# Kernel optimization log

Hardware: AMD Instinct MI355X
Metric: run time of the kernel (lower is better)

## Reference

```python
import jax, jax.numpy as jnp
import numpy as np

MEAN_STOP_TIME_S = 60.0
MIN_ROUTE_LEN = 2
DEMAND_TIME_WEIGHT = 0.5
ROUTE_TIME_WEIGHT = 0.5
UNSERVED_WEIGHT = 5.0

B, N, R, L, K = 64, 512, 40, 20, 4


def setup_inputs() -> dict:
    key = jax.random.key(0)
    ks = jax.random.split(key, 8)
    demand = jax.random.uniform(ks[0], (B, N, N), dtype=jnp.float32) * 10.0
    drive_times = jax.random.uniform(ks[1], (B, N, N), dtype=jnp.float32) * 1800.0
    transit_times = jax.random.uniform(ks[2], (B, N, N), dtype=jnp.float32) * 3600.0
    has_path = jax.random.randint(ks[3], (B, N, N), 0, 2) > 0
    n_transfers = jax.random.randint(ks[4], (B, N, N), 0, 4).astype(jnp.int32)
    # routes with -1 padding past a random per-route length
    routes = jax.random.randint(ks[5], (B, R, L), 0, N).astype(jnp.int32)
    lens = jax.random.randint(ks[6], (B, R), 0, L + 1)
    valid = jnp.arange(L)[None, None, :] < lens[:, :, None]
    batch_routes = jnp.where(valid, routes, -1)
    # per demand-edge route assignments, -1 = unused slot
    route_seqs = (jax.random.randint(ks[7], (B, N, N, K), 0, R + 1) - 1).astype(jnp.int32)
    return {
        'demand': demand, 'drive_times': drive_times, 'transit_times': transit_times,
        'has_path': has_path, 'n_transfers': n_transfers,
        'batch_routes': batch_routes, 'route_seqs': route_seqs,
    }


def _route_leg_times(batch_routes, dtm, mean_stop_time_s):
    # leg (l -> l+1) of each route: dtm[b, from, to] + stop time, masked on valid stops
    frm = batch_routes[:, :, :-1]
    to = batch_routes[:, :, 1:]
    valid = (frm >= 0) & (to >= 0)
    bidx = jnp.arange(dtm.shape[0])[:, None, None]
    times = dtm[bidx, jnp.maximum(frm, 0), jnp.maximum(to, 0)] + mean_stop_time_s
    return jnp.where(valid, times, 0.0)  # [B, R, L-1]


def _per_route_riders(demand, route_seqs, n_routes):
    # segment-sum demand over route ids; -1 slots go to a dump bucket
    def per_b(dem, rs):
        ids = rs.reshape(-1)
        vals = jnp.broadcast_to(dem[..., None], rs.shape).reshape(-1)
        ids = jnp.where(ids < 0, n_routes, ids)
        return jax.ops.segment_sum(vals, ids, num_segments=n_routes + 1)[:n_routes]
    return jax.vmap(per_b)(demand, route_seqs)  # [B, R]


def reference(demand, drive_times, transit_times, has_path, n_transfers,
              batch_routes, route_seqs):
    fdem = demand
    nopath = ~has_path
    route_lens = (batch_routes > -1).sum(-1)  # [B, R]

    n_disconnected = (nopath & (fdem > 0)).sum(axis=(1, 2))
    route_len_delta = jnp.maximum(MIN_ROUTE_LEN - route_lens, 0)
    route_len_delta = jnp.where(route_lens == 0, 0, route_len_delta)
    n_stops_oob = route_len_delta.sum(-1)  # [B]

    nt_eff = jnp.where(nopath, 3, n_transfers)
    tat = jnp.stack([
        (fdem * (nt_eff == 0)).sum(axis=(1, 2)),
        (fdem * (nt_eff == 1)).sum(axis=(1, 2)),
        (fdem * (nt_eff == 2)).sum(axis=(1, 2)),
        (fdem * (nt_eff > 2)).sum(axis=(1, 2)),
    ], axis=-1)  # trips_at_transfers [B, 4]

    trip_times = jnp.where(nopath, 0.0, transit_times)
    total_dmd_time = (fdem * trip_times).sum(axis=(1, 2))
    total_transfers = (fdem * n_transfers.astype(fdem.dtype)).sum(axis=(1, 2))
    unserved = (fdem * nopath).sum(axis=(1, 2))
    total_demand = fdem.sum(axis=(1, 2))

    leg_times = _route_leg_times(batch_routes, drive_times, MEAN_STOP_TIME_S)
    total_route_time = leg_times.sum(axis=(1, 2))
    # symmetric_routes=True: add return-direction legs
    ret = _route_leg_times(batch_routes, jnp.swapaxes(drive_times, 1, 2), MEAN_STOP_TIME_S)
    total_route_time = total_route_time + ret.sum(axis=(1, 2))

    per_route_riders = _per_route_riders(fdem, route_seqs, R)

    # cost assembly
    time_norm = drive_times.max(axis=(1, 2))
    served = total_demand - unserved
    mean_dmd_time = total_dmd_time / (served + 1e-6)
    norm_dmd_time = mean_dmd_time / time_norm
    n_routes_used = (route_lens > 0).sum(-1)
    norm_route_time = total_route_time / (time_norm * n_routes_used + 1e-6)
    n_demand_edges = (fdem > 0).sum(axis=(1, 2))
    frac_uncovered = n_disconnected / n_demand_edges
    denom = n_routes_used * MIN_ROUTE_LEN
    frac_oob = n_stops_oob / (denom + 1e-6)
    cost = (DEMAND_TIME_WEIGHT * norm_dmd_time
            + ROUTE_TIME_WEIGHT * norm_route_time
            + UNSERVED_WEIGHT * (frac_uncovered + frac_oob))
    return cost, per_route_riders, tat, total_route_time


if __name__ == '__main__':
    out = reference(**setup_inputs())
    print([o.shape for o in out])
```

## Files before the change

kernel.cpp:

```cpp
#include <hip/hip_runtime.h>

#define NB 64
#define NDIM 512
#define NNE (NDIM * NDIM)
#define NR 40
#define NL 20
#define SUBS 16
#define IT 16
#define BINS 41

#define K1OFF 0
#define K1STRIDE 16
#define K2OFF (NB * SUBS * K1STRIDE)
#define K3OFF (K2OFF + NB * SUBS)
#define K3STRIDE 48
#define RT_OFF (K3OFF + NB * SUBS * K3STRIDE)
#define FLAG_OFF (RT_OFF + NB * 4)

__global__ void detect_kernel(const unsigned int* __restrict__ hp, int* __restrict__ flag) {
    unsigned int v = hp[threadIdx.x];
    unsigned long long m = __ballot(v > 1u);
    if (threadIdx.x == 0) *flag = (m != 0ull) ? 1 : 0;
}

template<bool BYTE>
__device__ __forceinline__ void k1loop(const float* __restrict__ pd,
                                       const float* __restrict__ pt,
                                       const int* __restrict__ pn,
                                       const void* __restrict__ ph,
                                       float acc[9])
{
#pragma unroll 4
    for (int it = 0; it < IT; ++it) {
        const int o = it * 1024;
        const float4 dem = *(const float4*)(pd + o);
        const float4 tt  = *(const float4*)(pt + o);
        const int4   nt  = *(const int4*)(pn + o);
        int h[4];
        if (BYTE) {
            const uchar4 hb = *(const uchar4*)((const unsigned char*)ph + o);
            h[0] = hb.x; h[1] = hb.y; h[2] = hb.z; h[3] = hb.w;
        } else {
            const int4 hw = *(const int4*)((const int*)ph + o);
            h[0] = hw.x; h[1] = hw.y; h[2] = hw.z; h[3] = hw.w;
        }
        const float dm[4] = {dem.x, dem.y, dem.z, dem.w};
        const float tv[4] = {tt.x, tt.y, tt.z, tt.w};
        const int   nv[4] = {nt.x, nt.y, nt.z, nt.w};
#pragma unroll
        for (int e = 0; e < 4; ++e) {
            const float d = dm[e];
            const bool np_ = (h[e] == 0);
            const int nte = np_ ? 3 : nv[e];
            acc[0] += (nte == 0) ? d : 0.0f;
            acc[1] += (nte == 1) ? d : 0.0f;
            acc[2] += (nte == 2) ? d : 0.0f;
            acc[3] += (nte > 2) ? d : 0.0f;
            acc[4] += np_ ? 0.0f : d * tv[e];
            acc[5] += np_ ? d : 0.0f;
            acc[6] += d;
            const bool pos = d > 0.0f;
            acc[7] += (np_ && pos) ? 1.0f : 0.0f;
            acc[8] += pos ? 1.0f : 0.0f;
        }
    }
}

__global__ __launch_bounds__(256) void k1_kernel(
    const float* __restrict__ demand,
    const float* __restrict__ transit,
    const int* __restrict__ ntr,
    const unsigned char* __restrict__ hp_raw,
    const int* __restrict__ flag,
    float* __restrict__ ws)
{
    __shared__ float red[4][9];
    const int tid = threadIdx.x;
    const int wave = tid >> 6, lane = tid & 63;
    const int b = blockIdx.x >> 4, sub = blockIdx.x & 15;
    const size_t e0 = (size_t)b * NNE + (size_t)sub * (NNE / SUBS) + (size_t)tid * 4;

    float acc[9] = {0, 0, 0, 0, 0, 0, 0, 0, 0};
    if (*flag != 0)
        k1loop<true>(demand + e0, transit + e0, ntr + e0, hp_raw + e0, acc);
    else
        k1loop<false>(demand + e0, transit + e0, ntr + e0, ((const int*)hp_raw) + e0, acc);

#pragma unroll
    for (int o = 32; o > 0; o >>= 1)
#pragma unroll
        for (int v = 0; v < 9; ++v) acc[v] += __shfl_down(acc[v], o);
    if (lane == 0)
#pragma unroll
        for (int v = 0; v < 9; ++v) red[wave][v] = acc[v];
    __syncthreads();
    if (tid < 9)
        ws[K1OFF + (size_t)blockIdx.x * K1STRIDE + tid] =
            red[0][tid] + red[1][tid] + red[2][tid] + red[3][tid];
}

__global__ __launch_bounds__(256) void k2_kernel(
    const float* __restrict__ drive, float* __restrict__ ws)
{
    __shared__ float red[4];
    const int tid = threadIdx.x;
    const int wave = tid >> 6, lane = tid & 63;
    const int b = blockIdx.x >> 4, sub = blockIdx.x & 15;
    const float* p = drive + (size_t)b * NNE + (size_t)sub * (NNE / SUBS) + (size_t)tid * 4;

    float m0 = 0, m1 = 0, m2 = 0, m3 = 0;
#pragma unroll 4
    for (int it = 0; it < IT; ++it) {
        const float4 v = *(const float4*)(p + it * 1024);
        m0 = fmaxf(m0, v.x); m1 = fmaxf(m1, v.y);
        m2 = fmaxf(m2, v.z); m3 = fmaxf(m3, v.w);
    }
    float m = fmaxf(fmaxf(m0, m1), fmaxf(m2, m3));
#pragma unroll
    for (int o = 32; o > 0; o >>= 1) m = fmaxf(m, __shfl_down(m, o));
    if (lane == 0) red[wave] = m;
    __syncthreads();
    if (tid == 0)
        ws[K2OFF + blockIdx.x] = fmaxf(fmaxf(red[0], red[1]), fmaxf(red[2], red[3]));
}

__global__ __launch_bounds__(256) void k3_kernel(
    const float* __restrict__ demand,
    const int* __restrict__ rseq,
    float* __restrict__ ws)
{
    __shared__ float bins[256 * BINS];
    const int tid = threadIdx.x;
    float* __restrict__ myrow = bins + tid * BINS;
#pragma unroll
    for (int i = 0; i < BINS; ++i) myrow[i] = 0.0f;

    const int b = blockIdx.x >> 4, sub = blockIdx.x & 15;
    const size_t e0 = (size_t)b * NNE + (size_t)sub * (NNE / SUBS) + (size_t)tid * 4;
    const float* pd = demand + e0;
    const int* pr = rseq + e0 * 4;

#pragma unroll 2
    for (int it = 0; it < IT; ++it) {
        const int o = it * 1024;
        const float4 dem = *(const float4*)(pd + o);
        const int4 r0 = *(const int4*)(pr + o * 4);
        const int4 r1 = *(const int4*)(pr + o * 4 + 4);
        const int4 r2 = *(const int4*)(pr + o * 4 + 8);
        const int4 r3 = *(const int4*)(pr + o * 4 + 12);
        const float dm[4] = {dem.x, dem.y, dem.z, dem.w};
        const int rs[16] = {r0.x, r0.y, r0.z, r0.w, r1.x, r1.y, r1.z, r1.w,
                            r2.x, r2.y, r2.z, r2.w, r3.x, r3.y, r3.z, r3.w};
#pragma unroll
        for (int e = 0; e < 4; ++e) {
            const float d = dm[e];
#pragma unroll
            for (int k = 0; k < 4; ++k) {
                const unsigned row = min((unsigned)rs[e * 4 + k], (unsigned)(BINS - 1));
                myrow[row] += d;
            }
        }
    }
    __syncthreads();

    if (tid < NR) {
        float s = 0.0f;
        for (int r = 0; r < 256; ++r) s += bins[r * BINS + tid];
        ws[K3OFF + (size_t)blockIdx.x * K3STRIDE + tid] = s;
    }
}

__global__ __launch_bounds__(64) void route_kernel(
    const int* __restrict__ routes,
    const float* __restrict__ drive,
    float* __restrict__ ws)
{
    const int b = blockIdx.x;
    const int r = threadIdx.x;
    float t = 0.0f, used = 0.0f, oob = 0.0f;
    if (r < NR) {
        const int* rt = routes + (b * NR + r) * NL;
        int v[NL];
        int len = 0;
#pragma unroll
        for (int l = 0; l < NL; ++l) { v[l] = rt[l]; len += (v[l] > -1) ? 1 : 0; }
        const float* D = drive + (size_t)b * NNE;
#pragma unroll
        for (int l = 0; l < NL - 1; ++l) {
            int f = v[l], to = v[l + 1];
            if (f >= 0 && to >= 0)
                t += D[f * NDIM + to] + D[to * NDIM + f] + 120.0f;
        }
        used = (len > 0) ? 1.0f : 0.0f;
        int delta = 2 - len;
        oob = (len > 0 && delta > 0) ? (float)delta : 0.0f;
    }
#pragma unroll
    for (int o = 32; o > 0; o >>= 1) {
        t += __shfl_down(t, o);
        used += __shfl_down(used, o);
        oob += __shfl_down(oob, o);
    }
    if (r == 0) {
        float* a = ws + RT_OFF + b * 4;
        a[0] = t; a[1] = used; a[2] = oob;
    }
}

__global__ __launch_bounds__(64) void final_kernel(const float* __restrict__ ws,
                                                   float* __restrict__ out) {
    __shared__ float fin[50];
    const int b = blockIdx.x;
    const int v = threadIdx.x;
    if (v < 9) {
        float a = 0.0f;
#pragma unroll
        for (int s = 0; s < SUBS; ++s)
            a += ws[K1OFF + (size_t)(b * SUBS + s) * K1STRIDE + v];
        fin[v] = a;
    } else if (v == 9) {
        float m = 0.0f;
#pragma unroll
        for (int s = 0; s < SUBS; ++s)
            m = fmaxf(m, ws[K2OFF + b * SUBS + s]);
        fin[9] = m;
    } else if (v < 50) {
        float a = 0.0f;
#pragma unroll
        for (int s = 0; s < SUBS; ++s)
            a += ws[K3OFF + (size_t)(b * SUBS + s) * K3STRIDE + (v - 10)];
        fin[v] = a;
    }
    __syncthreads();
    if (v == 0) {
        const float* rt = ws + RT_OFF + b * 4;
        const float trt = rt[0], nru = rt[1], noob = rt[2];
        const float dmdt = fin[4], uns = fin[5], tdem = fin[6];
        const float ndisc = fin[7], nedge = fin[8], tn = fin[9];
        const float served = tdem - uns;
        const float cost = 0.5f * ((dmdt / (served + 1e-6f)) / tn)
                         + 0.5f * (trt / (tn * nru + 1e-6f))
                         + 5.0f * (ndisc / nedge + noob / (nru * 2.0f + 1e-6f));
        out[b] = cost;
        out[64 + NB * NR + NB * 4 + b] = trt;
    }
    if (v < 4) out[64 + NB * NR + b * 4 + v] = fin[v];
    if (v >= 10 && v < 50) out[64 + b * NR + (v - 10)] = fin[v];
}

extern "C" void kernel_launch(void* const* d_in, const int* in_sizes, int n_in,
                              void* d_out, int out_size, void* d_ws, size_t ws_size,
                              hipStream_t stream) {
    const float* demand  = (const float*)d_in[0];
    const float* drive   = (const float*)d_in[1];
    const float* transit = (const float*)d_in[2];
    const unsigned char* hp = (const unsigned char*)d_in[3];
    const int* ntr    = (const int*)d_in[4];
    const int* routes = (const int*)d_in[5];
    const int* rseq   = (const int*)d_in[6];
    float* out = (float*)d_out;
    float* ws  = (float*)d_ws;
    int* flag  = (int*)(ws + FLAG_OFF);

    detect_kernel<<<1, 64, 0, stream>>>((const unsigned int*)hp, flag);
    route_kernel<<<NB, 64, 0, stream>>>(routes, drive, ws);
    k1_kernel<<<NB * SUBS, 256, 0, stream>>>(demand, transit, ntr, hp, flag, ws);
    k2_kernel<<<NB * SUBS, 256, 0, stream>>>(drive, ws);
    k3_kernel<<<NB * SUBS, 256, 0, stream>>>(demand, rseq, ws);
    final_kernel<<<NB, 64, 0, stream>>>(ws, out);
}
```

Baseline: 151.2 us.

## Fuse stats, drive-max and route histogram kernels into one streaming pass

Merges the three full-grid passes (demand/transit statistics, drive-time max, per-route rider histogram) into a single kernel, so demand is read once instead of twice and two launches go away. The workspace layout becomes one 64-float stripe per block, and the final reduction is simplified to match. The fused kernel now carries the large shared-memory bin array alongside more live registers, which can limit occupancy (launch bounds request 3 blocks per SM).

Measured after the change: 137.8 us. 1.1x faster.

```diff
diff --git a/kernel.cpp b/kernel.cpp
--- a/kernel.cpp
+++ b/kernel.cpp
@@ -9,12 +9,8 @@
 #define IT 16
 #define BINS 41
 
-#define K1OFF 0
-#define K1STRIDE 16
-#define K2OFF (NB * SUBS * K1STRIDE)
-#define K3OFF (K2OFF + NB * SUBS)
-#define K3STRIDE 48
-#define RT_OFF (K3OFF + NB * SUBS * K3STRIDE)
+#define MAIN_STRIDE 64
+#define RT_OFF (NB * SUBS * MAIN_STRIDE)
 #define FLAG_OFF (RT_OFF + NB * 4)
 
 __global__ void detect_kernel(const unsigned int* __restrict__ hp, int* __restrict__ flag) {
@@ -24,18 +20,23 @@
 }
 
 template<bool BYTE>
-__device__ __forceinline__ void k1loop(const float* __restrict__ pd,
-                                       const float* __restrict__ pt,
-                                       const int* __restrict__ pn,
-                                       const void* __restrict__ ph,
-                                       float acc[9])
+__device__ __forceinline__ void mloop(
+    const float* __restrict__ pd, const float* __restrict__ pt,
+    const float* __restrict__ pdr, const int* __restrict__ pn,
+    const void* __restrict__ ph, const int* __restrict__ pr,
+    float acc[10], float* __restrict__ myrow)
 {
-#pragma unroll 4
+#pragma unroll 2
     for (int it = 0; it < IT; ++it) {
         const int o = it * 1024;
         const float4 dem = *(const float4*)(pd + o);
         const float4 tt  = *(const float4*)(pt + o);
+        const float4 dt  = *(const float4*)(pdr + o);
         const int4   nt  = *(const int4*)(pn + o);
+        const int4 r0 = *(const int4*)(pr + o * 4);
+        const int4 r1 = *(const int4*)(pr + o * 4 + 4);
+        const int4 r2 = *(const int4*)(pr + o * 4 + 8);
+        const int4 r3 = *(const int4*)(pr + o * 4 + 12);
         int h[4];
         if (BYTE) {
             const uchar4 hb = *(const uchar4*)((const unsigned char*)ph + o);
@@ -46,7 +47,10 @@
         }
         const float dm[4] = {dem.x, dem.y, dem.z, dem.w};
         const float tv[4] = {tt.x, tt.y, tt.z, tt.w};
+        const float dv[4] = {dt.x, dt.y, dt.z, dt.w};
         const int   nv[4] = {nt.x, nt.y, nt.z, nt.w};
+        const int rs[16] = {r0.x, r0.y, r0.z, r0.w, r1.x, r1.y, r1.z, r1.w,
+                            r2.x, r2.y, r2.z, r2.w, r3.x, r3.y, r3.z, r3.w};
 #pragma unroll
         for (int e = 0; e < 4; ++e) {
             const float d = dm[e];
@@ -62,98 +66,7 @@
             const bool pos = d > 0.0f;
             acc[7] += (np_ && pos) ? 1.0f : 0.0f;
             acc[8] += pos ? 1.0f : 0.0f;
-        }
-    }
-}
-
-__global__ __launch_bounds__(256) void k1_kernel(
-    const float* __restrict__ demand,
-    const float* __restrict__ transit,
-    const int* __restrict__ ntr,
-    const unsigned char* __restrict__ hp_raw,
-    const int* __restrict__ flag,
-    float* __restrict__ ws)
-{
-    __shared__ float red[4][9];
-    const int tid = threadIdx.x;
-    const int wave = tid >> 6, lane = tid & 63;
-    const int b = blockIdx.x >> 4, sub = blockIdx.x & 15;
-    const size_t e0 = (size_t)b * NNE + (size_t)sub * (NNE / SUBS) + (size_t)tid * 4;
-
-    float acc[9] = {0, 0, 0, 0, 0, 0, 0, 0, 0};
-    if (*flag != 0)
-        k1loop<true>(demand + e0, transit + e0, ntr + e0, hp_raw + e0, acc);
-    else
-        k1loop<false>(demand + e0, transit + e0, ntr + e0, ((const int*)hp_raw) + e0, acc);
-
-#pragma unroll
-    for (int o = 32; o > 0; o >>= 1)
-#pragma unroll
-        for (int v = 0; v < 9; ++v) acc[v] += __shfl_down(acc[v], o);
-    if (lane == 0)
-#pragma unroll
-        for (int v = 0; v < 9; ++v) red[wave][v] = acc[v];
-    __syncthreads();
-    if (tid < 9)
-        ws[K1OFF + (size_t)blockIdx.x * K1STRIDE + tid] =
-            red[0][tid] + red[1][tid] + red[2][tid] + red[3][tid];
-}
-
-__global__ __launch_bounds__(256) void k2_kernel(
-    const float* __restrict__ drive, float* __restrict__ ws)
-{
-    __shared__ float red[4];
-    const int tid = threadIdx.x;
-    const int wave = tid >> 6, lane = tid & 63;
-    const int b = blockIdx.x >> 4, sub = blockIdx.x & 15;
-    const float* p = drive + (size_t)b * NNE + (size_t)sub * (NNE / SUBS) + (size_t)tid * 4;
-
-    float m0 = 0, m1 = 0, m2 = 0, m3 = 0;
-#pragma unroll 4
-    for (int it = 0; it < IT; ++it) {
-        const float4 v = *(const float4*)(p + it * 1024);
-        m0 = fmaxf(m0, v.x); m1 = fmaxf(m1, v.y);
-        m2 = fmaxf(m2, v.z); m3 = fmaxf(m3, v.w);
-    }
-    float m = fmaxf(fmaxf(m0, m1), fmaxf(m2, m3));
-#pragma unroll
-    for (int o = 32; o > 0; o >>= 1) m = fmaxf(m, __shfl_down(m, o));
-    if (lane == 0) red[wave] = m;
-    __syncthreads();
-    if (tid == 0)
-        ws[K2OFF + blockIdx.x] = fmaxf(fmaxf(red[0], red[1]), fmaxf(red[2], red[3]));
-}
-
-__global__ __launch_bounds__(256) void k3_kernel(
-    const float* __restrict__ demand,
-    const int* __restrict__ rseq,
-    float* __restrict__ ws)
-{
-    __shared__ float bins[256 * BINS];
-    const int tid = threadIdx.x;
-    float* __restrict__ myrow = bins + tid * BINS;
-#pragma unroll
-    for (int i = 0; i < BINS; ++i) myrow[i] = 0.0f;
-
-    const int b = blockIdx.x >> 4, sub = blockIdx.x & 15;
-    const size_t e0 = (size_t)b * NNE + (size_t)sub * (NNE / SUBS) + (size_t)tid * 4;
-    const float* pd = demand + e0;
-    const int* pr = rseq + e0 * 4;
-
-#pragma unroll 2
-    for (int it = 0; it < IT; ++it) {
-        const int o = it * 1024;
-        const float4 dem = *(const float4*)(pd + o);
-        const int4 r0 = *(const int4*)(pr + o * 4);
-        const int4 r1 = *(const int4*)(pr + o * 4 + 4);
-        const int4 r2 = *(const int4*)(pr + o * 4 + 8);
-        const int4 r3 = *(const int4*)(pr + o * 4 + 12);
-        const float dm[4] = {dem.x, dem.y, dem.z, dem.w};
-        const int rs[16] = {r0.x, r0.y, r0.z, r0.w, r1.x, r1.y, r1.z, r1.w,
-                            r2.x, r2.y, r2.z, r2.w, r3.x, r3.y, r3.z, r3.w};
-#pragma unroll
-        for (int e = 0; e < 4; ++e) {
-            const float d = dm[e];
+            acc[9] = fmaxf(acc[9], dv[e]);
 #pragma unroll
             for (int k = 0; k < 4; ++k) {
                 const unsigned row = min((unsigned)rs[e * 4 + k], (unsigned)(BINS - 1));
@@ -161,12 +74,59 @@
             }
         }
     }
+}
+
+__global__ __launch_bounds__(256, 3) void main_kernel(
+    const float* __restrict__ demand,
+    const float* __restrict__ transit,
+    const float* __restrict__ drive,
+    const int* __restrict__ ntr,
+    const unsigned char* __restrict__ hp_raw,
+    const int* __restrict__ rseq,
+    const int* __restrict__ flag,
+    float* __restrict__ ws)
+{
+    __shared__ float bins[256 * BINS];
+    __shared__ float red[4][10];
+    const int tid = threadIdx.x;
+    const int wave = tid >> 6, lane = tid & 63;
+    float* __restrict__ myrow = bins + tid * BINS;
+#pragma unroll
+    for (int i = 0; i < BINS; ++i) myrow[i] = 0.0f;
+
+    const int b = blockIdx.x >> 4, sub = blockIdx.x & 15;
+    const size_t e0 = (size_t)b * NNE + (size_t)sub * (NNE / SUBS) + (size_t)tid * 4;
+
+    float acc[10] = {0, 0, 0, 0, 0, 0, 0, 0, 0, 0};
+    if (*flag != 0)
+        mloop<true>(demand + e0, transit + e0, drive + e0, ntr + e0,
+                    hp_raw + e0, rseq + e0 * 4, acc, myrow);
+    else
+        mloop<false>(demand + e0, transit + e0, drive + e0, ntr + e0,
+                     ((const int*)hp_raw) + e0, rseq + e0 * 4, acc, myrow);
+
+#pragma unroll
+    for (int o = 32; o > 0; o >>= 1) {
+#pragma unroll
+        for (int v = 0; v < 9; ++v) acc[v] += __shfl_down(acc[v], o);
+        acc[9] = fmaxf(acc[9], __shfl_down(acc[9], o));
+    }
+    if (lane == 0)
+#pragma unroll
+        for (int v = 0; v < 10; ++v) red[wave][v] = acc[v];
     __syncthreads();
 
+    float* part = ws + (size_t)blockIdx.x * MAIN_STRIDE;
+    if (tid < 10) {
+        if (tid == 9)
+            part[9] = fmaxf(fmaxf(red[0][9], red[1][9]), fmaxf(red[2][9], red[3][9]));
+        else
+            part[tid] = red[0][tid] + red[1][tid] + red[2][tid] + red[3][tid];
+    }
     if (tid < NR) {
         float s = 0.0f;
         for (int r = 0; r < 256; ++r) s += bins[r * BINS + tid];
-        ws[K3OFF + (size_t)blockIdx.x * K3STRIDE + tid] = s;
+        part[10 + tid] = s;
     }
 }
 
@@ -212,23 +172,14 @@
     __shared__ float fin[50];
     const int b = blockIdx.x;
     const int v = threadIdx.x;
-    if (v < 9) {
-        float a = 0.0f;
-#pragma unroll
-        for (int s = 0; s < SUBS; ++s)
-            a += ws[K1OFF + (size_t)(b * SUBS + s) * K1STRIDE + v];
-        fin[v] = a;
-    } else if (v == 9) {
-        float m = 0.0f;
-#pragma unroll
-        for (int s = 0; s < SUBS; ++s)
-            m = fmaxf(m, ws[K2OFF + b * SUBS + s]);
-        fin[9] = m;
-    } else if (v < 50) {
-        float a = 0.0f;
-#pragma unroll
-        for (int s = 0; s < SUBS; ++s)
-            a += ws[K3OFF + (size_t)(b * SUBS + s) * K3STRIDE + (v - 10)];
+    if (v < 50) {
+        const float* p = ws + (size_t)b * SUBS * MAIN_STRIDE + v;
+        float a = p[0];
+#pragma unroll
+        for (int s = 1; s < SUBS; ++s) {
+            const float x = p[(size_t)s * MAIN_STRIDE];
+            a = (v == 9) ? fmaxf(a, x) : (a + x);
+        }
         fin[v] = a;
     }
     __syncthreads();
@@ -264,8 +215,6 @@
 
     detect_kernel<<<1, 64, 0, stream>>>((const unsigned int*)hp, flag);
     route_kernel<<<NB, 64, 0, stream>>>(routes, drive, ws);
-    k1_kernel<<<NB * SUBS, 256, 0, stream>>>(demand, transit, ntr, hp, flag, ws);
-    k2_kernel<<<NB * SUBS, 256, 0, stream>>>(drive, ws);
-    k3_kernel<<<NB * SUBS, 256, 0, stream>>>(demand, rseq, ws);
+    main_kernel<<<NB * SUBS, 256, 0, stream>>>(demand, transit, drive, ntr, hp, rseq, flag, ws);
     final_kernel<<<NB, 64, 0, stream>>>(ws, out);
 }
```
